# Performance work log

Measured on AMD Instinct MI355X. Metric: run time of the kernel, lower is better.

The kernel has to match this reference:

```python
import jax, jax.numpy as jnp
import numpy as np

B, T, D, H = 8, 1024, 1024, 16
HS = D // H
EPS = 1e-5


def setup_inputs() -> dict:
    key = jax.random.key(0)
    ks = jax.random.split(key, 8)
    w = lambda k, sh: (jax.random.normal(k, sh, jnp.float32) * 0.02)
    return {
        "x": jax.random.normal(ks[0], (B, T, D), jnp.float32),
        "Wq": w(ks[1], (D, D)),
        "Wk": w(ks[2], (D, D)),
        "Wv": w(ks[3], (D, D)),
        "Wo": w(ks[4], (D, D)),
        "bo": jnp.zeros((D,), jnp.float32),
        "W1": w(ks[5], (D, 4 * D)),
        "b1": jnp.zeros((4 * D,), jnp.float32),
        "W2": w(ks[6], (4 * D, D)),
        "b2": jnp.zeros((D,), jnp.float32),
        "ln1_g": jnp.ones((D,), jnp.float32),
        "ln1_b": jnp.zeros((D,), jnp.float32),
        "ln2_g": jnp.ones((D,), jnp.float32),
        "ln2_b": jnp.zeros((D,), jnp.float32),
    }


def _ln(y, g, b):
    m = y.mean(-1, keepdims=True)
    v = ((y - m) ** 2).mean(-1, keepdims=True)
    return (y - m) * jax.lax.rsqrt(v + EPS) * g + b


def reference(x, Wq, Wk, Wv, Wo, bo, W1, b1, W2, b2, ln1_g, ln1_b, ln2_g, ln2_b):
    Bx, Tx, Dx = x.shape
    h = _ln(x, ln1_g, ln1_b)
    # per-head projections (heads concatenated along columns of Wq/Wk/Wv)
    q = (h @ Wq).reshape(Bx, Tx, H, HS).transpose(0, 2, 1, 3)  # [B,H,T,hs]
    k = (h @ Wk).reshape(Bx, Tx, H, HS).transpose(0, 2, 1, 3)
    v = (h @ Wv).reshape(Bx, Tx, H, HS).transpose(0, 2, 1, 3)
    # NOTE: original scales by 1/sqrt(C) with C = d_model, not head_size
    wei = jnp.einsum("bhqd,bhkd->bhqk", q, k) / jnp.sqrt(jnp.float32(Dx))
    mask = jnp.tril(jnp.ones((Tx, Tx), bool))
    wei = jnp.where(mask, wei, -jnp.inf)
    wei = jax.nn.softmax(wei, axis=-1)
    att = jnp.einsum("bhqk,bhkd->bhqd", wei, v)
    att = att.transpose(0, 2, 1, 3).reshape(Bx, Tx, Dx)  # concat heads
    x = x + att @ Wo + bo
    h2 = _ln(x, ln2_g, ln2_b)
    x = x + jax.nn.relu(h2 @ W1 + b1) @ W2 + b2
    return x
```

## Files before the change

### kernel.cpp

```cpp
#include <hip/hip_runtime.h>
#include <stdint.h>
#include <stddef.h>

typedef unsigned short u16;
typedef u16 u16x4 __attribute__((ext_vector_type(4)));
typedef u16 u16x8 __attribute__((ext_vector_type(8)));
typedef __bf16 bf16x8 __attribute__((ext_vector_type(8)));
typedef float f32x4 __attribute__((ext_vector_type(4)));

__device__ __forceinline__ float b2f(u16 u) {
    return __uint_as_float(((unsigned)u) << 16);
}
__device__ __forceinline__ u16 f2b(float f) {
    unsigned u = __float_as_uint(f);
    u += 0x7FFF + ((u >> 16) & 1);
    return (u16)(u >> 16);
}
__device__ __forceinline__ bf16x8 bcast(u16x8 v) { return __builtin_bit_cast(bf16x8, v); }
__device__ __forceinline__ f32x4 mfma16(bf16x8 a, bf16x8 b, f32x4 c) {
    return __builtin_amdgcn_mfma_f32_16x16x32_bf16(a, b, c, 0, 0, 0);
}
typedef const __attribute__((address_space(1))) void* gas1;
typedef __attribute__((address_space(3))) void* las3;
__device__ __forceinline__ void gload_lds16(const void* g, void* l) {
    __builtin_amdgcn_global_load_lds((gas1)g, (las3)l, 16, 0, 0);
}

#define DPP_ROR_F32(x, N) __builtin_bit_cast(float, __builtin_amdgcn_update_dpp( \
    __builtin_bit_cast(int, (x)), __builtin_bit_cast(int, (x)), 0x120 + (N), 0xf, 0xf, false))
__device__ __forceinline__ float red_max16(float x) {
    x = fmaxf(x, DPP_ROR_F32(x, 8));
    x = fmaxf(x, DPP_ROR_F32(x, 4));
    x = fmaxf(x, DPP_ROR_F32(x, 2));
    x = fmaxf(x, DPP_ROR_F32(x, 1));
    return x;
}
__device__ __forceinline__ float red_add16(float x) {
    x += DPP_ROR_F32(x, 8);
    x += DPP_ROR_F32(x, 4);
    x += DPP_ROR_F32(x, 2);
    x += DPP_ROR_F32(x, 1);
    return x;
}

__global__ __launch_bounds__(256) void transpose_k(const float* __restrict__ in,
                                                   u16* __restrict__ out,
                                                   int R, int C) {
    __shared__ u16 t[32][33];
    int x = blockIdx.x * 32 + threadIdx.x;
    int y0 = blockIdx.y * 32;
#pragma unroll
    for (int j = threadIdx.y; j < 32; j += 8)
        t[j][threadIdx.x] = f2b(in[(size_t)(y0 + j) * C + x]);
    __syncthreads();
    int xo = y0 + threadIdx.x;
    int yo0 = blockIdx.x * 32;
#pragma unroll
    for (int j = threadIdx.y; j < 32; j += 8)
        out[(size_t)(yo0 + j) * R + xo] = t[threadIdx.x][j];
}

__global__ __launch_bounds__(256) void ln_k(const void* __restrict__ x,
                                            const float* __restrict__ g,
                                            const float* __restrict__ b,
                                            u16* __restrict__ y,
                                            int x_f32) {
    const int row = blockIdx.x;
    const size_t ro = (size_t)row * 1024;
    float v[4], s = 0.0f, ss = 0.0f;
#pragma unroll
    for (int i = 0; i < 4; ++i) {
        size_t idx = ro + threadIdx.x + i * 256;
        float f = x_f32 ? ((const float*)x)[idx] : b2f(((const u16*)x)[idx]);
        v[i] = f; s += f; ss += f * f;
    }
#pragma unroll
    for (int off = 32; off; off >>= 1) {
        s += __shfl_down(s, off);
        ss += __shfl_down(ss, off);
    }
    __shared__ float red[2][4];
    int wave = threadIdx.x >> 6, lane = threadIdx.x & 63;
    if (lane == 0) { red[0][wave] = s; red[1][wave] = ss; }
    __syncthreads();
    s = red[0][0] + red[0][1] + red[0][2] + red[0][3];
    ss = red[1][0] + red[1][1] + red[1][2] + red[1][3];
    float mean = s * (1.0f / 1024.0f);
    float var = ss * (1.0f / 1024.0f) - mean * mean;
    float inv = rsqrtf(var + 1e-5f);
#pragma unroll
    for (int i = 0; i < 4; ++i) {
        int c = threadIdx.x + i * 256;
        float o = (v[i] - mean) * inv * g[c] + b[c];
        y[ro + c] = f2b(o);
    }
}

__device__ __forceinline__ void gemm128_core(const u16* __restrict__ A,
                                             const u16* __restrict__ Bt,
                                             const int Ksz, const int m0,
                                             const int n0, u16* lds,
                                             f32x4 (&acc)[4][4]) {
    char* ldsb = (char*)lds;
    const int tid = threadIdx.x;
    const int w = tid >> 6, lane = tid & 63;
    const int quad = lane >> 4, l16 = lane & 15;
    const int wr = w >> 2, wc = w & 3;
    const int rS = w * 8 + (lane >> 3);
    const int cS = ((lane & 7) ^ (lane >> 3)) * 8;
    const int dstW = w * 1024;
    const int xo = (l16 & 7) << 4;
    const int co0 = (quad * 16) ^ xo;
    const int co1 = (64 + quad * 16) ^ xo;
    const int aoffB = wr * 8192 + l16 * 128;
    const int boffB = wc * 8192 + l16 * 128;
    const u16* pA = A + (size_t)(m0 + rS) * Ksz + cS;
    const u16* pB = Bt + (size_t)(n0 + rS) * Ksz + cS;
    const int nK = Ksz >> 6;
    const size_t rstep = (size_t)64 * Ksz;

#define STG_A(dd, kt) do { \
    const u16* _s = pA + (size_t)(kt) * 64; \
    char* _d = ldsb + (dd) * 16384 + dstW; \
    gload_lds16(_s, _d); \
    gload_lds16(_s + rstep, _d + 8192); \
} while (0)
#define STG_B(dd, h, kt) do { \
    const u16* _s = pB + (size_t)((h) * 128) * Ksz + (kt) * 64; \
    char* _d = ldsb + 32768 + (dd) * 32768 + (h) * 16384 + dstW; \
    gload_lds16(_s, _d); \
    gload_lds16(_s + rstep, _d + 8192); \
} while (0)

    bf16x8 af[2][4], bg[2][2][2];

#define LDA128() do { \
    _Pragma("unroll") for (int mi = 0; mi < 4; ++mi) { \
        af[0][mi] = bcast(*(const u16x8*)(ldsA + mi * 2048 + co0)); \
        af[1][mi] = bcast(*(const u16x8*)(ldsA + mi * 2048 + co1)); \
    } \
} while (0)
#define LDB128(nh) do { \
    _Pragma("unroll") for (int n2 = 0; n2 < 2; ++n2) { \
        bg[(nh)][0][n2] = bcast(*(const u16x8*)(ldsBp + ((nh) * 2 + n2) * 2048 + co0)); \
        bg[(nh)][1][n2] = bcast(*(const u16x8*)(ldsBp + ((nh) * 2 + n2) * 2048 + co1)); \
    } \
} while (0)
#define QUAD128(nh) do { \
    _Pragma("unroll") for (int mi = 0; mi < 4; ++mi) \
    _Pragma("unroll") for (int n2 = 0; n2 < 2; ++n2) { \
        acc[mi][(nh) * 2 + n2] = mfma16(af[0][mi], bg[(nh)][0][n2], acc[mi][(nh) * 2 + n2]); \
        acc[mi][(nh) * 2 + n2] = mfma16(af[1][mi], bg[(nh)][1][n2], acc[mi][(nh) * 2 + n2]); \
    } \
} while (0)

    STG_A(0, 0); STG_B(0, 0, 0); STG_B(0, 1, 0);
    asm volatile("s_waitcnt vmcnt(0)" ::: "memory");
    __builtin_amdgcn_s_barrier();
    asm volatile("" ::: "memory");

    for (int t = 0; t < nK; ++t) {
        const int d = t & 1, e = d ^ 1;
        const char* ldsA = ldsb + d * 16384 + aoffB;
        const char* ldsBp = ldsb + 32768 + d * 32768 + boffB;
        if (t + 1 < nK) { STG_A(e, t + 1); STG_B(e, 0, t + 1); STG_B(e, 1, t + 1); }
        LDA128(); LDB128(0);
        asm volatile("s_waitcnt lgkmcnt(0)" ::: "memory");
        __builtin_amdgcn_s_setprio(1);
        QUAD128(0);
        __builtin_amdgcn_s_setprio(0);
        LDB128(1);
        asm volatile("s_waitcnt lgkmcnt(0)" ::: "memory");
        __builtin_amdgcn_s_setprio(1);
        QUAD128(1);
        __builtin_amdgcn_s_setprio(0);
        asm volatile("s_waitcnt vmcnt(0)" ::: "memory");
        __builtin_amdgcn_s_barrier();
        asm volatile("" ::: "memory");
    }
#undef STG_A
#undef STG_B
#undef LDA128
#undef LDB128
#undef QUAD128
}

__global__ __launch_bounds__(512, 2) void gemm128(const u16* __restrict__ A,
                                                  const u16* __restrict__ Bt,
                                                  void* __restrict__ Cout,
                                                  int M, int N, int K,
                                                  const float* __restrict__ bias,
                                                  const void* __restrict__ resid,
                                                  int relu, int resid_f32, int out_f32) {
    (void)M;
    __shared__ __attribute__((aligned(16))) u16 lds[49152];
    f32x4 acc[4][4] = {};
    const int m0 = blockIdx.y * 128, n0 = blockIdx.x * 256;
    gemm128_core(A, Bt, K, m0, n0, lds, acc);
    const int tid = threadIdx.x;
    const int w = tid >> 6, lane = tid & 63;
    const int quad = lane >> 4, l16 = lane & 15;
    const int wr = w >> 2, wc = w & 3;
    const int row0 = m0 + wr * 64;
    if (out_f32) {
#pragma unroll
        for (int nj = 0; nj < 4; ++nj) {
            const int col = n0 + wc * 64 + nj * 16 + l16;
            const float bv = bias ? bias[col] : 0.0f;
#pragma unroll
            for (int mi = 0; mi < 4; ++mi) {
#pragma unroll
                for (int r = 0; r < 4; ++r) {
                    const size_t idx = (size_t)(row0 + mi * 16 + quad * 4 + r) * N + col;
                    float val = acc[mi][nj][r] + bv;
                    if (resid)
                        val += resid_f32 ? ((const float*)resid)[idx]
                                         : b2f(((const u16*)resid)[idx]);
                    if (relu) val = fmaxf(val, 0.0f);
                    ((float*)Cout)[idx] = val;
                }
            }
        }
    } else {
        u16* patch = &lds[w * 4608];
#pragma unroll
        for (int nj = 0; nj < 4; ++nj) {
            const int col = n0 + wc * 64 + nj * 16 + l16;
            const float bv = bias ? bias[col] : 0.0f;
#pragma unroll
            for (int mi = 0; mi < 4; ++mi) {
#pragma unroll
                for (int r = 0; r < 4; ++r) {
                    const int lr = mi * 16 + quad * 4 + r;
                    float val = acc[mi][nj][r] + bv;
                    if (resid) {
                        const size_t idx = (size_t)(row0 + lr) * N + col;
                        val += resid_f32 ? ((const float*)resid)[idx]
                                         : b2f(((const u16*)resid)[idx]);
                    }
                    if (relu) val = fmaxf(val, 0.0f);
                    patch[lr * 72 + nj * 16 + l16] = f2b(val);
                }
            }
        }
        asm volatile("s_waitcnt lgkmcnt(0)" ::: "memory");
        const int pr = lane >> 3, pc = (lane & 7) * 8;
        u16* gout = (u16*)Cout + (size_t)row0 * N + n0 + wc * 64;
#pragma unroll
        for (int p = 0; p < 8; ++p) {
            u16x8 v = *(const u16x8*)&patch[(p * 8 + pr) * 72 + pc];
            *(u16x8*)&gout[(size_t)(p * 8 + pr) * N + pc] = v;
        }
    }
}

__global__ __launch_bounds__(512, 2) void gemm128_qkv(const u16* __restrict__ A,
                                                      const u16* __restrict__ Bt,
                                                      u16* __restrict__ qb,
                                                      u16* __restrict__ kb,
                                                      u16* __restrict__ vbT) {
    __shared__ __attribute__((aligned(16))) u16 lds[49152];
    f32x4 acc[4][4] = {};
    const int m0 = blockIdx.y * 128, n0 = blockIdx.x * 256;
    gemm128_core(A, Bt, 1024, m0, n0, lds, acc);
    const int tid = threadIdx.x;
    const int w = tid >> 6, lane = tid & 63;
    const int quad = lane >> 4, l16 = lane & 15;
    const int wr = w >> 2, wc = w & 3;
    const int row0 = m0 + wr * 64;
    const int tens = blockIdx.x >> 2;
    const int nbase = (blockIdx.x & 3) * 256 + wc * 64;
    u16* patch = &lds[w * 4608];
    const int pr = lane >> 3, pc = (lane & 7) * 8;
    if (tens < 2) {
        u16* dst = tens ? kb : qb;
#pragma unroll
        for (int mi = 0; mi < 4; ++mi)
#pragma unroll
            for (int nj = 0; nj < 4; ++nj)
#pragma unroll
                for (int r = 0; r < 4; ++r)
                    patch[(mi * 16 + quad * 4 + r) * 72 + nj * 16 + l16] =
                        f2b(acc[mi][nj][r]);
        asm volatile("s_waitcnt lgkmcnt(0)" ::: "memory");
        u16* gout = dst + (size_t)row0 * 1024 + nbase;
#pragma unroll
        for (int p = 0; p < 8; ++p) {
            u16x8 v = *(const u16x8*)&patch[(p * 8 + pr) * 72 + pc];
            *(u16x8*)&gout[(size_t)(p * 8 + pr) * 1024 + pc] = v;
        }
    } else {
#pragma unroll
        for (int mi = 0; mi < 4; ++mi)
#pragma unroll
            for (int nj = 0; nj < 4; ++nj)
#pragma unroll
                for (int r = 0; r < 4; ++r)
                    patch[(nj * 16 + l16) * 72 + mi * 16 + quad * 4 + r] =
                        f2b(acc[mi][nj][r]);
        asm volatile("s_waitcnt lgkmcnt(0)" ::: "memory");
        const int b = row0 >> 10, t0 = row0 & 1023;
        const int h = nbase >> 6;
        u16* gout = vbT + (((size_t)(b * 16 + h) * 64) << 10) + t0;
#pragma unroll
        for (int p = 0; p < 8; ++p) {
            u16x8 v = *(const u16x8*)&patch[(p * 8 + pr) * 72 + pc];
            *(u16x8*)&gout[((size_t)(p * 8 + pr) << 10) + pc] = v;
        }
    }
}

__global__ __launch_bounds__(256) void attn_k(const u16* __restrict__ q,
                                              const u16* __restrict__ k,
                                              const u16* __restrict__ vt,
                                              u16* __restrict__ att) {
    __shared__ __attribute__((aligned(16))) u16 Ks[64][72];
    __shared__ __attribute__((aligned(16))) u16 Vts[64][72];
    __shared__ __attribute__((aligned(16))) u16 QP[128 * 72];
    const int qt = 7 - blockIdx.x;
    const int bh = blockIdx.y;
    const int bb = bh >> 4, hd = bh & 15;
    const int q0 = qt * 128;
    const size_t base  = (size_t)bb * 1024 * 1024 + (size_t)hd * 64;
    const size_t vbase = (size_t)bh << 16;
    const int tid = threadIdx.x;
    const int w = tid >> 6, lane = tid & 63;
    const int quad = lane >> 4, l16 = lane & 15;

#pragma unroll
    for (int it = 0; it < 4; ++it) {
        int f = it * 256 + tid;
        int r = f >> 3, c8 = (f & 7) * 8;
        *(u16x8*)&QP[r * 72 + c8] = *(const u16x8*)(q + base + (size_t)(q0 + r) * 1024 + c8);
    }
    __syncthreads();
    bf16x8 qf[2][2];
#pragma unroll
    for (int qi = 0; qi < 2; ++qi)
#pragma unroll
        for (int ks = 0; ks < 2; ++ks)
            qf[qi][ks] = bcast(*(const u16x8*)&QP[(w * 32 + qi * 16 + l16) * 72 + ks * 32 + quad * 8]);
    u16* Ps = &QP[(w * 32) * 72];

    f32x4 oacc[2][4] = {};
    float mrow[2][4], lrow[2][4];
#pragma unroll
    for (int qi = 0; qi < 2; ++qi)
#pragma unroll
        for (int r = 0; r < 4; ++r) { mrow[qi][r] = -1e30f; lrow[qi][r] = 0.0f; }

    const int njt = qt * 2 + 2;
    for (int jt = 0; jt < njt; ++jt) {
        const int j0 = jt * 64;
#pragma unroll
        for (int it = 0; it < 2; ++it) {
            int f = it * 256 + tid;
            int r = f >> 3, c8 = (f & 7) * 8;
            *(u16x8*)&Ks[r][c8]  = *(const u16x8*)(k  + base  + (size_t)(j0 + r) * 1024 + c8);
            *(u16x8*)&Vts[r][c8] = *(const u16x8*)(vt + vbase + (size_t)r * 1024 + j0 + c8);
        }
        __syncthreads();

        f32x4 s[2][4] = {};
#pragma unroll
        for (int kj = 0; kj < 4; ++kj) {
            bf16x8 b0 = bcast(*(const u16x8*)&Ks[kj * 16 + l16][quad * 8]);
            bf16x8 b1 = bcast(*(const u16x8*)&Ks[kj * 16 + l16][32 + quad * 8]);
#pragma unroll
            for (int qi = 0; qi < 2; ++qi) {
                s[qi][kj] = mfma16(qf[qi][0], b0, s[qi][kj]);
                s[qi][kj] = mfma16(qf[qi][1], b1, s[qi][kj]);
            }
        }

        float tmax[2][4], alpha[2][4], rs[2][4];
#pragma unroll
        for (int qi = 0; qi < 2; ++qi)
#pragma unroll
            for (int r = 0; r < 4; ++r) {
                const int qrow = q0 + w * 32 + qi * 16 + quad * 4 + r;
                float tm = -1e30f;
#pragma unroll
                for (int kj = 0; kj < 4; ++kj) {
                    const int col = j0 + kj * 16 + l16;
                    float sv = s[qi][kj][r] * 0.03125f;
                    sv = (col > qrow) ? -1e30f : sv;
                    s[qi][kj][r] = sv;
                    tm = fmaxf(tm, sv);
                }
                tmax[qi][r] = tm;
            }
#pragma unroll
        for (int qi = 0; qi < 2; ++qi)
#pragma unroll
            for (int r = 0; r < 4; ++r)
                tmax[qi][r] = red_max16(tmax[qi][r]);
#pragma unroll
        for (int qi = 0; qi < 2; ++qi)
#pragma unroll
            for (int r = 0; r < 4; ++r) {
                float mnew = fmaxf(mrow[qi][r], tmax[qi][r]);
                alpha[qi][r] = __expf(mrow[qi][r] - mnew);
                mrow[qi][r] = mnew;
                float accp = 0.0f;
#pragma unroll
                for (int kj = 0; kj < 4; ++kj) {
                    float p = __expf(s[qi][kj][r] - mnew);
                    s[qi][kj][r] = p;
                    accp += p;
                }
                rs[qi][r] = accp;
            }
#pragma unroll
        for (int qi = 0; qi < 2; ++qi)
#pragma unroll
            for (int r = 0; r < 4; ++r)
                rs[qi][r] = red_add16(rs[qi][r]);
#pragma unroll
        for (int qi = 0; qi < 2; ++qi)
#pragma unroll
            for (int r = 0; r < 4; ++r) {
                lrow[qi][r] = lrow[qi][r] * alpha[qi][r] + rs[qi][r];
#pragma unroll
                for (int oj = 0; oj < 4; ++oj) oacc[qi][oj][r] *= alpha[qi][r];
            }
#pragma unroll
        for (int qi = 0; qi < 2; ++qi)
#pragma unroll
            for (int r = 0; r < 4; ++r)
#pragma unroll
                for (int kj = 0; kj < 4; ++kj)
                    Ps[(qi * 16 + quad * 4 + r) * 72 + kj * 16 + l16] = f2b(s[qi][kj][r]);

#pragma unroll
        for (int ks = 0; ks < 2; ++ks) {
            bf16x8 a0 = bcast(*(const u16x8*)&Ps[(l16) * 72 + ks * 32 + quad * 8]);
            bf16x8 a1 = bcast(*(const u16x8*)&Ps[(16 + l16) * 72 + ks * 32 + quad * 8]);
#pragma unroll
            for (int oj = 0; oj < 4; ++oj) {
                bf16x8 bv = bcast(*(const u16x8*)&Vts[oj * 16 + l16][ks * 32 + quad * 8]);
                oacc[0][oj] = mfma16(a0, bv, oacc[0][oj]);
                oacc[1][oj] = mfma16(a1, bv, oacc[1][oj]);
            }
        }
        __syncthreads();
    }
#pragma unroll
    for (int qi = 0; qi < 2; ++qi)
#pragma unroll
        for (int oj = 0; oj < 4; ++oj)
#pragma unroll
            for (int r = 0; r < 4; ++r) {
                int row = q0 + w * 32 + qi * 16 + quad * 4 + r;
                float o = oacc[qi][oj][r] / lrow[qi][r];
                att[base + (size_t)row * 1024 + oj * 16 + l16] = f2b(o);
            }
}

extern "C" void kernel_launch(void* const* d_in, const int* in_sizes, int n_in,
                              void* d_out, int out_size, void* d_ws, size_t ws_size,
                              hipStream_t stream) {
    (void)in_sizes; (void)n_in; (void)out_size;
    const float* x   = (const float*)d_in[0];
    const float* Wq  = (const float*)d_in[1];
    const float* Wk  = (const float*)d_in[2];
    const float* Wv  = (const float*)d_in[3];
    const float* Wo  = (const float*)d_in[4];
    const float* bo  = (const float*)d_in[5];
    const float* W1  = (const float*)d_in[6];
    const float* b1  = (const float*)d_in[7];
    const float* W2  = (const float*)d_in[8];
    const float* b2  = (const float*)d_in[9];
    const float* g1  = (const float*)d_in[10];
    const float* be1 = (const float*)d_in[11];
    const float* g2  = (const float*)d_in[12];
    const float* be2 = (const float*)d_in[13];
    float* out = (float*)d_out;

    u16* ws = (u16*)d_ws;
    const size_t MIO = 1024u * 1024u;
    u16* Wt0 = ws;
    u16* Wt1 = ws + 4 * MIO;
    u16* qb  = ws + 8 * MIO;
    u16* kb  = ws + 16 * MIO;
    u16* vb  = ws + 24 * MIO;
    u16* mid = ws + 32 * MIO;
    u16* hb  = (u16*)d_out;
    const int full_ffn = ws_size >= (size_t)64 * MIO * 2;

    dim3 tb32(32, 8);

    ln_k<<<8192, 256, 0, stream>>>(x, g1, be1, hb, 1);

    transpose_k<<<dim3(32, 32), tb32, 0, stream>>>(Wq, Wt0,           1024, 1024);
    transpose_k<<<dim3(32, 32), tb32, 0, stream>>>(Wk, Wt0 + 1 * MIO, 1024, 1024);
    transpose_k<<<dim3(32, 32), tb32, 0, stream>>>(Wv, Wt0 + 2 * MIO, 1024, 1024);
    gemm128_qkv<<<dim3(12, 64), 512, 0, stream>>>(hb, Wt0, qb, kb, vb);

    attn_k<<<dim3(8, 128), 256, 0, stream>>>(qb, kb, vb, hb);

    transpose_k<<<dim3(32, 32), tb32, 0, stream>>>(Wo, Wt1, 1024, 1024);
    gemm128<<<dim3(4, 64), 512, 0, stream>>>(hb, Wt1, qb, 8192, 1024, 1024, bo, x, 0, 1, 0);

    ln_k<<<8192, 256, 0, stream>>>(qb, g2, be2, kb, 0);

    transpose_k<<<dim3(128, 32), tb32, 0, stream>>>(W1, Wt0, 1024, 4096);
    transpose_k<<<dim3(32, 128), tb32, 0, stream>>>(W2, Wt1, 4096, 1024);
    if (full_ffn) {
        gemm128<<<dim3(16, 64), 512, 0, stream>>>(kb, Wt0, mid, 8192, 4096, 1024, b1, nullptr, 1, 0, 0);
        gemm128<<<dim3(4, 64), 512, 0, stream>>>(mid, Wt1, out, 8192, 1024, 4096, b2, qb, 0, 0, 1);
    } else {
        for (int c = 0; c < 4; ++c) {
            const size_t ro = (size_t)c * 2048 * 1024;
            gemm128<<<dim3(16, 16), 512, 0, stream>>>(kb + ro, Wt0, vb, 2048, 4096, 1024, b1, nullptr, 1, 0, 0);
            gemm128<<<dim3(4, 16), 512, 0, stream>>>(vb, Wt1, out + ro, 2048, 1024, 4096, b2, qb + ro, 0, 0, 1);
        }
    }
}
```

Before: 562.9 us.

## Pair causal query tiles per attention block and skip unneeded mask/rescale work

Each attention block now handles two query tiles (qt and 7-qt), so every block does the same amount of causal work, and the grid shrinks from 8 to 4 blocks along x. The causal mask is applied only on diagonal key tiles. The online-softmax rescale of the accumulators is skipped when no row maximum in the wavefront increased. This targets load imbalance across blocks and some VALU work, at the cost of half as many blocks, which means lower occupancy and longer serial work per block.

Result: faster. 532.1 us (-5.5%).

```diff
diff --git a/kernel.cpp b/kernel.cpp
--- a/kernel.cpp
+++ b/kernel.cpp
@@ -317,144 +317,187 @@
     __shared__ __attribute__((aligned(16))) u16 Ks[64][72];
     __shared__ __attribute__((aligned(16))) u16 Vts[64][72];
     __shared__ __attribute__((aligned(16))) u16 QP[128 * 72];
-    const int qt = 7 - blockIdx.x;
     const int bh = blockIdx.y;
     const int bb = bh >> 4, hd = bh & 15;
-    const int q0 = qt * 128;
     const size_t base  = (size_t)bb * 1024 * 1024 + (size_t)hd * 64;
     const size_t vbase = (size_t)bh << 16;
     const int tid = threadIdx.x;
     const int w = tid >> 6, lane = tid & 63;
     const int quad = lane >> 4, l16 = lane & 15;
-
-#pragma unroll
-    for (int it = 0; it < 4; ++it) {
-        int f = it * 256 + tid;
-        int r = f >> 3, c8 = (f & 7) * 8;
-        *(u16x8*)&QP[r * 72 + c8] = *(const u16x8*)(q + base + (size_t)(q0 + r) * 1024 + c8);
-    }
-    __syncthreads();
-    bf16x8 qf[2][2];
-#pragma unroll
-    for (int qi = 0; qi < 2; ++qi)
-#pragma unroll
-        for (int ks = 0; ks < 2; ++ks)
-            qf[qi][ks] = bcast(*(const u16x8*)&QP[(w * 32 + qi * 16 + l16) * 72 + ks * 32 + quad * 8]);
     u16* Ps = &QP[(w * 32) * 72];
 
-    f32x4 oacc[2][4] = {};
-    float mrow[2][4], lrow[2][4];
-#pragma unroll
-    for (int qi = 0; qi < 2; ++qi)
-#pragma unroll
-        for (int r = 0; r < 4; ++r) { mrow[qi][r] = -1e30f; lrow[qi][r] = 0.0f; }
-
-    const int njt = qt * 2 + 2;
-    for (int jt = 0; jt < njt; ++jt) {
-        const int j0 = jt * 64;
-#pragma unroll
-        for (int it = 0; it < 2; ++it) {
+    for (int half = 0; half < 2; ++half) {
+        const int qt = half ? blockIdx.x : 7 - blockIdx.x;
+        const int q0 = qt * 128;
+        __syncthreads();
+
+#pragma unroll
+        for (int it = 0; it < 4; ++it) {
             int f = it * 256 + tid;
             int r = f >> 3, c8 = (f & 7) * 8;
-            *(u16x8*)&Ks[r][c8]  = *(const u16x8*)(k  + base  + (size_t)(j0 + r) * 1024 + c8);
-            *(u16x8*)&Vts[r][c8] = *(const u16x8*)(vt + vbase + (size_t)r * 1024 + j0 + c8);
+            *(u16x8*)&QP[r * 72 + c8] = *(const u16x8*)(q + base + (size_t)(q0 + r) * 1024 + c8);
         }
         __syncthreads();
-
-        f32x4 s[2][4] = {};
-#pragma unroll
-        for (int kj = 0; kj < 4; ++kj) {
-            bf16x8 b0 = bcast(*(const u16x8*)&Ks[kj * 16 + l16][quad * 8]);
-            bf16x8 b1 = bcast(*(const u16x8*)&Ks[kj * 16 + l16][32 + quad * 8]);
-#pragma unroll
-            for (int qi = 0; qi < 2; ++qi) {
-                s[qi][kj] = mfma16(qf[qi][0], b0, s[qi][kj]);
-                s[qi][kj] = mfma16(qf[qi][1], b1, s[qi][kj]);
-            }
-        }
-
-        float tmax[2][4], alpha[2][4], rs[2][4];
+        bf16x8 qf[2][2];
 #pragma unroll
         for (int qi = 0; qi < 2; ++qi)
 #pragma unroll
-            for (int r = 0; r < 4; ++r) {
-                const int qrow = q0 + w * 32 + qi * 16 + quad * 4 + r;
-                float tm = -1e30f;
-#pragma unroll
-                for (int kj = 0; kj < 4; ++kj) {
-                    const int col = j0 + kj * 16 + l16;
-                    float sv = s[qi][kj][r] * 0.03125f;
-                    sv = (col > qrow) ? -1e30f : sv;
-                    s[qi][kj][r] = sv;
-                    tm = fmaxf(tm, sv);
+            for (int ks = 0; ks < 2; ++ks)
+                qf[qi][ks] = bcast(*(const u16x8*)&QP[(w * 32 + qi * 16 + l16) * 72 + ks * 32 + quad * 8]);
+
+        f32x4 oacc[2][4] = {};
+        float mrow[2][4], lrow[2][4];
+#pragma unroll
+        for (int qi = 0; qi < 2; ++qi)
+#pragma unroll
+            for (int r = 0; r < 4; ++r) { mrow[qi][r] = -1e30f; lrow[qi][r] = 0.0f; }
+
+        const int njt = qt * 2 + 2;
+        for (int jt = 0; jt < njt; ++jt) {
+            const int j0 = jt * 64;
+#pragma unroll
+            for (int it = 0; it < 2; ++it) {
+                int f = it * 256 + tid;
+                int r = f >> 3, c8 = (f & 7) * 8;
+                *(u16x8*)&Ks[r][c8]  = *(const u16x8*)(k  + base  + (size_t)(j0 + r) * 1024 + c8);
+                *(u16x8*)&Vts[r][c8] = *(const u16x8*)(vt + vbase + (size_t)r * 1024 + j0 + c8);
+            }
+            __syncthreads();
+
+            f32x4 s[2][4] = {};
+#pragma unroll
+            for (int kj = 0; kj < 4; ++kj) {
+                bf16x8 b0 = bcast(*(const u16x8*)&Ks[kj * 16 + l16][quad * 8]);
+                bf16x8 b1 = bcast(*(const u16x8*)&Ks[kj * 16 + l16][32 + quad * 8]);
+#pragma unroll
+                for (int qi = 0; qi < 2; ++qi) {
+                    s[qi][kj] = mfma16(qf[qi][0], b0, s[qi][kj]);
+                    s[qi][kj] = mfma16(qf[qi][1], b1, s[qi][kj]);
                 }
-                tmax[qi][r] = tm;
-            }
+            }
+
+            float tmax[2][4], alpha[2][4], rs[2][4];
+            if (jt >= 2 * qt) {
+#pragma unroll
+                for (int qi = 0; qi < 2; ++qi)
+#pragma unroll
+                    for (int r = 0; r < 4; ++r) {
+                        const int qrow = q0 + w * 32 + qi * 16 + quad * 4 + r;
+                        float tm = -1e30f;
+#pragma unroll
+                        for (int kj = 0; kj < 4; ++kj) {
+                            const int col = j0 + kj * 16 + l16;
+                            float sv = s[qi][kj][r] * 0.03125f;
+                            sv = (col > qrow) ? -1e30f : sv;
+                            s[qi][kj][r] = sv;
+                            tm = fmaxf(tm, sv);
+                        }
+                        tmax[qi][r] = tm;
+                    }
+            } else {
+#pragma unroll
+                for (int qi = 0; qi < 2; ++qi)
+#pragma unroll
+                    for (int r = 0; r < 4; ++r) {
+                        float tm = -1e30f;
+#pragma unroll
+                        for (int kj = 0; kj < 4; ++kj) {
+                            float sv = s[qi][kj][r] * 0.03125f;
+                            s[qi][kj][r] = sv;
+                            tm = fmaxf(tm, sv);
+                        }
+                        tmax[qi][r] = tm;
+                    }
+            }
+#pragma unroll
+            for (int qi = 0; qi < 2; ++qi)
+#pragma unroll
+                for (int r = 0; r < 4; ++r)
+                    tmax[qi][r] = red_max16(tmax[qi][r]);
+            int grow = 0;
+#pragma unroll
+            for (int qi = 0; qi < 2; ++qi)
+#pragma unroll
+                for (int r = 0; r < 4; ++r)
+                    grow |= (tmax[qi][r] > mrow[qi][r]) ? 1 : 0;
+            const bool rescale = __any(grow);
+            if (rescale) {
+#pragma unroll
+                for (int qi = 0; qi < 2; ++qi)
+#pragma unroll
+                    for (int r = 0; r < 4; ++r) {
+                        float mnew = fmaxf(mrow[qi][r], tmax[qi][r]);
+                        alpha[qi][r] = __expf(mrow[qi][r] - mnew);
+                        mrow[qi][r] = mnew;
+                    }
+            }
+#pragma unroll
+            for (int qi = 0; qi < 2; ++qi)
+#pragma unroll
+                for (int r = 0; r < 4; ++r) {
+                    const float m = mrow[qi][r];
+                    float accp = 0.0f;
+#pragma unroll
+                    for (int kj = 0; kj < 4; ++kj) {
+                        float p = __expf(s[qi][kj][r] - m);
+                        s[qi][kj][r] = p;
+                        accp += p;
+                    }
+                    rs[qi][r] = accp;
+                }
+#pragma unroll
+            for (int qi = 0; qi < 2; ++qi)
+#pragma unroll
+                for (int r = 0; r < 4; ++r)
+                    rs[qi][r] = red_add16(rs[qi][r]);
+            if (rescale) {
+#pragma unroll
+                for (int qi = 0; qi < 2; ++qi)
+#pragma unroll
+                    for (int r = 0; r < 4; ++r) {
+                        lrow[qi][r] = lrow[qi][r] * alpha[qi][r] + rs[qi][r];
+#pragma unroll
+                        for (int oj = 0; oj < 4; ++oj) oacc[qi][oj][r] *= alpha[qi][r];
+                    }
+            } else {
+#pragma unroll
+                for (int qi = 0; qi < 2; ++qi)
+#pragma unroll
+                    for (int r = 0; r < 4; ++r)
+                        lrow[qi][r] += rs[qi][r];
+            }
+#pragma unroll
+            for (int qi = 0; qi < 2; ++qi)
+#pragma unroll
+                for (int r = 0; r < 4; ++r)
+#pragma unroll
+                    for (int kj = 0; kj < 4; ++kj)
+                        Ps[(qi * 16 + quad * 4 + r) * 72 + kj * 16 + l16] = f2b(s[qi][kj][r]);
+
+#pragma unroll
+            for (int ks = 0; ks < 2; ++ks) {
+                bf16x8 a0 = bcast(*(const u16x8*)&Ps[(l16) * 72 + ks * 32 + quad * 8]);
+                bf16x8 a1 = bcast(*(const u16x8*)&Ps[(16 + l16) * 72 + ks * 32 + quad * 8]);
+#pragma unroll
+                for (int oj = 0; oj < 4; ++oj) {
+                    bf16x8 bv = bcast(*(const u16x8*)&Vts[oj * 16 + l16][ks * 32 + quad * 8]);
+                    oacc[0][oj] = mfma16(a0, bv, oacc[0][oj]);
+                    oacc[1][oj] = mfma16(a1, bv, oacc[1][oj]);
+                }
+            }
+            __syncthreads();
+        }
 #pragma unroll
         for (int qi = 0; qi < 2; ++qi)
 #pragma unroll
-            for (int r = 0; r < 4; ++r)
-                tmax[qi][r] = red_max16(tmax[qi][r]);
-#pragma unroll
-        for (int qi = 0; qi < 2; ++qi)
-#pragma unroll
-            for (int r = 0; r < 4; ++r) {
-                float mnew = fmaxf(mrow[qi][r], tmax[qi][r]);
-                alpha[qi][r] = __expf(mrow[qi][r] - mnew);
-                mrow[qi][r] = mnew;
-                float accp = 0.0f;
-#pragma unroll
-                for (int kj = 0; kj < 4; ++kj) {
-                    float p = __expf(s[qi][kj][r] - mnew);
-                    s[qi][kj][r] = p;
-                    accp += p;
+            for (int oj = 0; oj < 4; ++oj)
+#pragma unroll
+                for (int r = 0; r < 4; ++r) {
+                    int row = q0 + w * 32 + qi * 16 + quad * 4 + r;
+                    float o = oacc[qi][oj][r] / lrow[qi][r];
+                    att[base + (size_t)row * 1024 + oj * 16 + l16] = f2b(o);
                 }
-                rs[qi][r] = accp;
-            }
-#pragma unroll
-        for (int qi = 0; qi < 2; ++qi)
-#pragma unroll
-            for (int r = 0; r < 4; ++r)
-                rs[qi][r] = red_add16(rs[qi][r]);
-#pragma unroll
-        for (int qi = 0; qi < 2; ++qi)
-#pragma unroll
-            for (int r = 0; r < 4; ++r) {
-                lrow[qi][r] = lrow[qi][r] * alpha[qi][r] + rs[qi][r];
-#pragma unroll
-                for (int oj = 0; oj < 4; ++oj) oacc[qi][oj][r] *= alpha[qi][r];
-            }
-#pragma unroll
-        for (int qi = 0; qi < 2; ++qi)
-#pragma unroll
-            for (int r = 0; r < 4; ++r)
-#pragma unroll
-                for (int kj = 0; kj < 4; ++kj)
-                    Ps[(qi * 16 + quad * 4 + r) * 72 + kj * 16 + l16] = f2b(s[qi][kj][r]);
-
-#pragma unroll
-        for (int ks = 0; ks < 2; ++ks) {
-            bf16x8 a0 = bcast(*(const u16x8*)&Ps[(l16) * 72 + ks * 32 + quad * 8]);
-            bf16x8 a1 = bcast(*(const u16x8*)&Ps[(16 + l16) * 72 + ks * 32 + quad * 8]);
-#pragma unroll
-            for (int oj = 0; oj < 4; ++oj) {
-                bf16x8 bv = bcast(*(const u16x8*)&Vts[oj * 16 + l16][ks * 32 + quad * 8]);
-                oacc[0][oj] = mfma16(a0, bv, oacc[0][oj]);
-                oacc[1][oj] = mfma16(a1, bv, oacc[1][oj]);
-            }
-        }
-        __syncthreads();
-    }
-#pragma unroll
-    for (int qi = 0; qi < 2; ++qi)
-#pragma unroll
-        for (int oj = 0; oj < 4; ++oj)
-#pragma unroll
-            for (int r = 0; r < 4; ++r) {
-                int row = q0 + w * 32 + qi * 16 + quad * 4 + r;
-                float o = oacc[qi][oj][r] / lrow[qi][r];
-                att[base + (size_t)row * 1024 + oj * 16 + l16] = f2b(o);
-            }
+    }
 }
 
 extern "C" void kernel_launch(void* const* d_in, const int* in_sizes, int n_in,
@@ -497,7 +540,7 @@
     transpose_k<<<dim3(32, 32), tb32, 0, stream>>>(Wv, Wt0 + 2 * MIO, 1024, 1024);
     gemm128_qkv<<<dim3(12, 64), 512, 0, stream>>>(hb, Wt0, qb, kb, vb);
 
-    attn_k<<<dim3(8, 128), 256, 0, stream>>>(qb, kb, vb, hb);
+    attn_k<<<dim3(4, 128), 256, 0, stream>>>(qb, kb, vb, hb);
 
     transpose_k<<<dim3(32, 32), tb32, 0, stream>>>(Wo, Wt1, 1024, 1024);
     gemm128<<<dim3(4, 64), 512, 0, stream>>>(hb, Wt1, qb, 8192, 1024, 1024, bo, x, 0, 1, 0);
```
